# Kernel tuning notes

Measured on AMD Instinct MI355X. Metric: run time of the kernel, lower is better.

The kernel has to match this reference:

```python
import jax, jax.numpy as jnp
import numpy as np

T, E, D, F, K, CAP = 4096, 8, 1024, 4096, 2, 1024


def setup_inputs() -> dict:
    key = jax.random.key(0)
    ks = jax.random.split(key, 4)
    x = jax.random.normal(ks[0], (T, D), jnp.float32)
    # top-k routing: mask/weight consistent with a softmax router
    logits = jax.random.normal(ks[1], (T, E), jnp.float32)
    probs = jax.nn.softmax(logits, axis=-1)
    _, topi = jax.lax.top_k(probs, K)  # (T, K)
    route_mask = jnp.zeros((T, E), jnp.bool_).at[jnp.arange(T)[:, None], topi].set(True)
    route_weight = jnp.where(route_mask, probs, 0.0)
    # stacked expert MLP params (E leading axis, as ModuleGroup stacks them)
    w1 = jax.random.normal(ks[2], (E, D, F), jnp.float32) * 0.02
    b1 = jnp.zeros((E, F), jnp.float32)
    w2 = jax.random.normal(ks[3], (E, F, D), jnp.float32) * 0.02
    b2 = jnp.zeros((E, D), jnp.float32)
    return dict(x=x, route_mask=route_mask, route_weight=route_weight,
                w1=w1, b1=b1, w2=w2, b2=b2)


def _build_slots(mask_te, w_te, cap):
    # mask_te: (T,E) bool; w_te: (T,E) float (0 where unrouted)
    Tn, En = mask_te.shape
    m_et = mask_te.T                              # (E,T)
    w_et = jnp.where(m_et, w_te.T, -jnp.inf)      # unrouted -> -inf
    _, idx_top = jax.lax.top_k(w_et, cap)         # (E,C) token ids per slot
    slot = jnp.zeros((En, cap, Tn), w_te.dtype)
    slot = slot.at[jnp.arange(En)[:, None], jnp.arange(cap)[None, :], idx_top].set(1.0)
    slot = slot * m_et[:, None, :].astype(w_te.dtype)  # zero slots from -inf picks
    # NOTE: the original re-orders slots along C (a stable sort); the combine
    # einsum sums over C so the output is invariant to slot order -- skipped.
    return slot


def reference(x, route_mask, route_weight, w1, b1, w2, b2):
    w_te = jnp.where(route_mask, route_weight, 0.0)      # (T,E)
    slot = _build_slots(route_mask, w_te, CAP)           # (E,C,T) one-hot
    # dispatch: 'ect,t...->ec...'
    xs = jnp.einsum('ect,td->ecd', slot, x)              # (E,C,D)
    # expert compute (vmapped MLP over E)
    h = jax.nn.gelu(jnp.einsum('ecd,edf->ecf', xs, w1) + b1[:, None, :])
    out = jnp.einsum('ecf,efd->ecd', h, w2) + b2[:, None, :]
    # combine: 'ecf,ect,te->tf'
    y = jnp.einsum('ecd,ect,te->td', out, slot, w_te)    # (T,D)
    return y
```

## Files before the change

kernel.cpp:

```cpp
#include <hip/hip_runtime.h>
#include <hip/hip_bf16.h>
#include <stdint.h>

#define T_TOK 4096
#define E_EXP 8
#define D_DIM 1024
#define F_DIM 4096
#define K_TOP 2
#define CAPC  1024

typedef __attribute__((ext_vector_type(8))) short short8;
typedef __attribute__((ext_vector_type(4))) float f32x4;
typedef __attribute__((ext_vector_type(4))) unsigned short u16x4;

static __device__ __forceinline__ unsigned short f2bf(float f) {
  union { float f; unsigned u; } v; v.f = f;
  unsigned r = v.u + 0x7fffu + ((v.u >> 16) & 1u);
  return (unsigned short)(r >> 16);
}

static __device__ __forceinline__ void gload_lds16(const void* g, void* l) {
  __builtin_amdgcn_global_load_lds(
      (const __attribute__((address_space(1))) unsigned int*)g,
      (__attribute__((address_space(3))) unsigned int*)l, 16, 0, 0);
}

__global__ void zero_int_kernel(int* p, int n) {
  int i = blockIdx.x * 256 + threadIdx.x;
  if (i < n) p[i] = 0;
}

__global__ __launch_bounds__(1024) void select_kernel(
    const float* __restrict__ rw,
    int* __restrict__ sel_idx,
    int* __restrict__ inv_cnt,
    int* __restrict__ inv_ec,
    float* __restrict__ inv_w)
{
  __shared__ unsigned keys[T_TOK];
  __shared__ int hist[256];
  __shared__ int scan_s[1024];
  __shared__ int sh_need;
  __shared__ unsigned sh_prefix;
  __shared__ int slot_ctr;
  const int e = blockIdx.x;
  const int tid = threadIdx.x;

  if (tid < CAPC) sel_idx[e * CAPC + tid] = -1;
#pragma unroll
  for (int j = 0; j < 4; ++j) {
    int t = tid * 4 + j;
    float w = rw[(size_t)t * E_EXP + e];
    keys[t] = (w > 0.f) ? __float_as_uint(w) : 0u;
  }
  if (tid == 0) slot_ctr = 0;

  int need = CAPC;
  unsigned prefix = 0;
  for (int shift = 24; shift >= 0; shift -= 8) {
    __syncthreads();
    if (tid < 256) hist[tid] = 0;
    __syncthreads();
#pragma unroll
    for (int j = 0; j < 4; ++j) {
      unsigned k = keys[tid * 4 + j];
      unsigned hi = (shift == 24) ? 0u : (k >> (shift + 8));
      if (hi == prefix) atomicAdd(&hist[(k >> shift) & 255u], 1);
    }
    __syncthreads();
    if (tid == 0) {
      int cum = 0, b = 0;
      for (b = 255; b >= 0; --b) {
        cum += hist[b];
        if (cum >= need) break;
      }
      if (b < 0) b = 0;
      sh_need = need - (cum - hist[b]);
      sh_prefix = (prefix << 8) | (unsigned)b;
    }
    __syncthreads();
    need = sh_need;
    prefix = sh_prefix;
  }
  const unsigned thr = prefix;
  __syncthreads();

  int eqflag[4], myeq = 0;
#pragma unroll
  for (int j = 0; j < 4; ++j) {
    const int t = tid * 4 + j;
    const unsigned k = keys[t];
    if (k > thr) {
      int s = atomicAdd(&slot_ctr, 1);
      sel_idx[e * CAPC + s] = t;
      int p = atomicAdd(&inv_cnt[t], 1);
      inv_ec[t * K_TOP + p] = e * CAPC + s;
      inv_w[t * K_TOP + p] = __uint_as_float(k);
    }
    eqflag[j] = (thr > 0u && k == thr) ? 1 : 0;
    myeq += eqflag[j];
  }
  scan_s[tid] = myeq;
  __syncthreads();
  for (int d = 1; d < 1024; d <<= 1) {
    int v = scan_s[tid];
    int add = (tid >= d) ? scan_s[tid - d] : 0;
    __syncthreads();
    scan_s[tid] = v + add;
    __syncthreads();
  }
  int r = scan_s[tid] - myeq;
  const int base = CAPC - need;
#pragma unroll
  for (int j = 0; j < 4; ++j) {
    if (eqflag[j]) {
      if (r < need) {
        const int t = tid * 4 + j;
        const int s = base + r;
        sel_idx[e * CAPC + s] = t;
        int p = atomicAdd(&inv_cnt[t], 1);
        inv_ec[t * K_TOP + p] = e * CAPC + s;
        inv_w[t * K_TOP + p] = __uint_as_float(thr);
      }
      ++r;
    }
  }
}

__global__ void convert_x_kernel(const float* __restrict__ x,
                                 unsigned short* __restrict__ xb, int n4) {
  int i = blockIdx.x * 256 + threadIdx.x;
  if (i >= n4) return;
  f32x4 v = ((const f32x4*)x)[i];
  u16x4 o = { f2bf(v.x), f2bf(v.y), f2bf(v.z), f2bf(v.w) };
  ((u16x4*)xb)[i] = o;
}

__global__ __launch_bounds__(256) void transpose_bf16_kernel(
    const float* __restrict__ in, unsigned short* __restrict__ out,
    int R, int C)
{
  __shared__ unsigned short tile[64][68];
  const int e = blockIdx.z;
  const float* inp = in + (size_t)e * R * C;
  unsigned short* outp = out + (size_t)e * R * C;
  const int c0 = blockIdx.x * 64, r0 = blockIdx.y * 64;
  const int q4 = (threadIdx.x & 15) * 4;
  const int tr = threadIdx.x >> 4;
  for (int rr = tr; rr < 64; rr += 16) {
    f32x4 v = *(const f32x4*)(inp + (size_t)(r0 + rr) * C + c0 + q4);
    tile[rr][q4 + 0] = f2bf(v.x);
    tile[rr][q4 + 1] = f2bf(v.y);
    tile[rr][q4 + 2] = f2bf(v.z);
    tile[rr][q4 + 3] = f2bf(v.w);
  }
  __syncthreads();
  for (int cc = tr; cc < 64; cc += 16) {
    u16x4 o = { tile[q4 + 0][cc], tile[q4 + 1][cc],
                tile[q4 + 2][cc], tile[q4 + 3][cc] };
    *(u16x4*)(outp + (size_t)(c0 + cc) * R + r0 + q4) = o;
  }
}


__global__ __launch_bounds__(256, 3) void gemm1_kernel(
    const unsigned short* __restrict__ xb,
    const int* __restrict__ sel_idx,
    const unsigned short* __restrict__ w1t,
    const float* __restrict__ b1,
    unsigned short* __restrict__ H)
{
  const int lin = blockIdx.x + 32 * (blockIdx.y + 8 * blockIdx.z);
  const int e = lin & 7;
  const int slot = lin >> 3;
  const int xb_ = slot >> 3;
  const int yb_ = slot & 7;
  const int m0 = yb_ * 128;
  const int n0 = xb_ * 128;

  __shared__ __align__(16) unsigned short Asm[128 * 64];
  __shared__ __align__(16) unsigned short Bsm[128 * 64];
  const int tid = threadIdx.x;
  const int lane = tid & 63, wv = tid >> 6;
  const int wm = (wv >> 1) * 64, wn = (wv & 1) * 64;
  const int lrow = lane & 15, quad = lane >> 4;

  const int rbase = tid >> 3, seg = tid & 7;
  const int cs = seg ^ (rbase & 7);
  const unsigned short* gA[4];
  const unsigned short* gB[4];
  char* lA[4];
  char* lB[4];
  const unsigned short* w1e = w1t + (size_t)e * F_DIM * D_DIM;
#pragma unroll
  for (int it = 0; it < 4; ++it) {
    const int row = rbase + it * 32;
    int t = sel_idx[e * CAPC + m0 + row];
    if (t < 0) t = 0;
    gA[it] = xb + (size_t)t * D_DIM + cs * 8;
    gB[it] = w1e + (size_t)(n0 + row) * D_DIM + cs * 8;
    lA[it] = (char*)Asm + it * 4096 + wv * 1024;
    lB[it] = (char*)Bsm + it * 4096 + wv * 1024;
  }

  f32x4 acc[4][4];
#pragma unroll
  for (int a = 0; a < 4; ++a)
#pragma unroll
    for (int b = 0; b < 4; ++b) acc[a][b] = (f32x4){0.f, 0.f, 0.f, 0.f};

  const int sw = lrow & 7;
  for (int k0 = 0; k0 < D_DIM; k0 += 64) {
#pragma unroll
    for (int it = 0; it < 4; ++it) { gload_lds16(gA[it], lA[it]); gA[it] += 64; }
#pragma unroll
    for (int it = 0; it < 4; ++it) { gload_lds16(gB[it], lB[it]); gB[it] += 64; }
    __syncthreads();
#pragma unroll
    for (int h = 0; h < 2; ++h) {
      short8 af[4], bf[4];
#pragma unroll
      for (int mt = 0; mt < 4; ++mt)
        af[mt] = *(const short8*)(Asm + (wm + mt * 16 + lrow) * 64 +
                                  (((h << 2) + quad) ^ sw) * 8);
#pragma unroll
      for (int nt = 0; nt < 4; ++nt)
        bf[nt] = *(const short8*)(Bsm + (wn + nt * 16 + lrow) * 64 +
                                  (((h << 2) + quad) ^ sw) * 8);
#pragma unroll
      for (int mt = 0; mt < 4; ++mt)
#pragma unroll
        for (int nt = 0; nt < 4; ++nt)
          acc[mt][nt] = __builtin_amdgcn_mfma_f32_16x16x32_bf16(
              af[mt], bf[nt], acc[mt][nt], 0, 0, 0);
    }
    __syncthreads();
  }

  const float* b1e = b1 + e * F_DIM;
#pragma unroll
  for (int nt = 0; nt < 4; ++nt) {
    const int col = n0 + wn + nt * 16 + lrow;
    const float bias = b1e[col];
#pragma unroll
    for (int mt = 0; mt < 4; ++mt) {
      const int rowb = m0 + wm + mt * 16 + quad * 4;
#pragma unroll
      for (int i = 0; i < 4; ++i) {
        float v = acc[mt][nt][i] + bias;
        float u = 0.7978845608028654f * (v + 0.044715f * v * v * v);
        float th = 1.f - 2.f / (1.f + __expf(2.f * u));
        float hv = 0.5f * v * (1.f + th);
        H[((size_t)e * CAPC + rowb + i) * F_DIM + col] = f2bf(hv);
      }
    }
  }
}

__global__ __launch_bounds__(256, 3) void gemm2_kernel(
    const unsigned short* __restrict__ H,
    const unsigned short* __restrict__ w2t,
    const float* __restrict__ b2,
    float* __restrict__ P)
{
  const int lin = blockIdx.x + 8 * (blockIdx.y + 8 * blockIdx.z);
  const int xcd = lin & 7;
  const int slot = lin >> 3;
  const int g = xcd * 2 + (slot >> 6);
  const int e = g & 7;
  const int ks = g >> 3;
  const int tile = slot & 63;
  const int xb_ = tile >> 3;
  const int yb_ = tile & 7;
  const int m0 = yb_ * 128;
  const int n0 = xb_ * 128;
  const int kbase = ks * (F_DIM / 2);

  __shared__ __align__(16) unsigned short Asm[128 * 64];
  __shared__ __align__(16) unsigned short Bsm[128 * 64];
  const int tid = threadIdx.x;
  const int lane = tid & 63, wv = tid >> 6;
  const int wm = (wv >> 1) * 64, wn = (wv & 1) * 64;
  const int lrow = lane & 15, quad = lane >> 4;

  const int rbase = tid >> 3, seg = tid & 7;
  const int cs = seg ^ (rbase & 7);
  const unsigned short* gA[4];
  const unsigned short* gB[4];
  char* lA[4];
  char* lB[4];
  const unsigned short* He = H + (size_t)e * CAPC * F_DIM;
  const unsigned short* w2e = w2t + (size_t)e * D_DIM * F_DIM;
#pragma unroll
  for (int it = 0; it < 4; ++it) {
    const int row = rbase + it * 32;
    gA[it] = He + (size_t)(m0 + row) * F_DIM + kbase + cs * 8;
    gB[it] = w2e + (size_t)(n0 + row) * F_DIM + kbase + cs * 8;
    lA[it] = (char*)Asm + it * 4096 + wv * 1024;
    lB[it] = (char*)Bsm + it * 4096 + wv * 1024;
  }

  f32x4 acc[4][4];
#pragma unroll
  for (int a = 0; a < 4; ++a)
#pragma unroll
    for (int b = 0; b < 4; ++b) acc[a][b] = (f32x4){0.f, 0.f, 0.f, 0.f};

  const int sw = lrow & 7;
  for (int k0 = 0; k0 < F_DIM / 2; k0 += 64) {
#pragma unroll
    for (int it = 0; it < 4; ++it) { gload_lds16(gA[it], lA[it]); gA[it] += 64; }
#pragma unroll
    for (int it = 0; it < 4; ++it) { gload_lds16(gB[it], lB[it]); gB[it] += 64; }
    __syncthreads();
#pragma unroll
    for (int h = 0; h < 2; ++h) {
      short8 af[4], bf[4];
#pragma unroll
      for (int mt = 0; mt < 4; ++mt)
        af[mt] = *(const short8*)(Asm + (wm + mt * 16 + lrow) * 64 +
                                  (((h << 2) + quad) ^ sw) * 8);
#pragma unroll
      for (int nt = 0; nt < 4; ++nt)
        bf[nt] = *(const short8*)(Bsm + (wn + nt * 16 + lrow) * 64 +
                                  (((h << 2) + quad) ^ sw) * 8);
#pragma unroll
      for (int mt = 0; mt < 4; ++mt)
#pragma unroll
        for (int nt = 0; nt < 4; ++nt)
          acc[mt][nt] = __builtin_amdgcn_mfma_f32_16x16x32_bf16(
              af[mt], bf[nt], acc[mt][nt], 0, 0, 0);
    }
    __syncthreads();
  }

  const float* b2e = b2 + e * D_DIM;
  float* Pk = P + (size_t)ks * E_EXP * CAPC * D_DIM;
#pragma unroll
  for (int nt = 0; nt < 4; ++nt) {
    const int col = n0 + wn + nt * 16 + lrow;
    const float bias = (ks == 0) ? b2e[col] : 0.f;
#pragma unroll
    for (int mt = 0; mt < 4; ++mt) {
      const int rowb = m0 + wm + mt * 16 + quad * 4;
#pragma unroll
      for (int i = 0; i < 4; ++i) {
        Pk[((size_t)e * CAPC + rowb + i) * D_DIM + col] = acc[mt][nt][i] + bias;
      }
    }
  }
}

__global__ __launch_bounds__(256) void combine_kernel(
    const float* __restrict__ P, const int* __restrict__ inv_cnt,
    const int* __restrict__ inv_ec, const float* __restrict__ inv_w,
    float* __restrict__ y)
{
  const int t = blockIdx.x;
  const int cnt = inv_cnt[t];
  f32x4 s = {0.f, 0.f, 0.f, 0.f};
  const int d4 = threadIdx.x;
  const size_t half = (size_t)E_EXP * CAPC * D_DIM;
  for (int p = 0; p < cnt; ++p) {
    const int ec = inv_ec[t * K_TOP + p];
    const float w = inv_w[t * K_TOP + p];
    f32x4 v0 = ((const f32x4*)(P + (size_t)ec * D_DIM))[d4];
    f32x4 v1 = ((const f32x4*)(P + half + (size_t)ec * D_DIM))[d4];
    s += (v0 + v1) * w;
  }
  ((f32x4*)(y + (size_t)t * D_DIM))[d4] = s;
}

extern "C" void kernel_launch(void* const* d_in, const int* in_sizes, int n_in,
                              void* d_out, int out_size, void* d_ws, size_t ws_size,
                              hipStream_t stream) {
  (void)in_sizes; (void)n_in; (void)out_size; (void)ws_size;
  const float* x  = (const float*)d_in[0];
  const float* rw = (const float*)d_in[2];
  const float* w1 = (const float*)d_in[3];
  const float* b1 = (const float*)d_in[4];
  const float* w2 = (const float*)d_in[5];
  const float* b2 = (const float*)d_in[6];
  float* y = (float*)d_out;

  char* ws = (char*)d_ws;
  size_t off = 0;
  auto alloc = [&](size_t bytes) {
    void* p = ws + off;
    off += (bytes + 255) & ~(size_t)255;
    return p;
  };
  unsigned short* xb  = (unsigned short*)alloc((size_t)T_TOK * D_DIM * 2);
  unsigned short* w1t = (unsigned short*)alloc((size_t)E_EXP * F_DIM * D_DIM * 2);
  unsigned short* w2t = (unsigned short*)alloc((size_t)E_EXP * D_DIM * F_DIM * 2);
  unsigned short* H   = (unsigned short*)alloc((size_t)E_EXP * CAPC * F_DIM * 2);
  float* P            = (float*)alloc((size_t)2 * E_EXP * CAPC * D_DIM * 4);
  int* sel_idx        = (int*)alloc((size_t)E_EXP * CAPC * 4);
  int* inv_cnt        = (int*)alloc((size_t)T_TOK * 4);
  int* inv_ec         = (int*)alloc((size_t)T_TOK * K_TOP * 4);
  float* inv_w        = (float*)alloc((size_t)T_TOK * K_TOP * 4);

  zero_int_kernel<<<(T_TOK + 255) / 256, 256, 0, stream>>>(inv_cnt, T_TOK);
  select_kernel<<<E_EXP, 1024, 0, stream>>>(rw, sel_idx, inv_cnt, inv_ec, inv_w);

  convert_x_kernel<<<(T_TOK * D_DIM / 4 + 255) / 256, 256, 0, stream>>>(
      x, xb, T_TOK * D_DIM / 4);
  transpose_bf16_kernel<<<dim3(F_DIM / 64, D_DIM / 64, E_EXP), 256, 0, stream>>>(
      w1, w1t, D_DIM, F_DIM);
  transpose_bf16_kernel<<<dim3(D_DIM / 64, F_DIM / 64, E_EXP), 256, 0, stream>>>(
      w2, w2t, F_DIM, D_DIM);

  gemm1_kernel<<<dim3(F_DIM / 128, CAPC / 128, E_EXP), 256, 0, stream>>>(
      xb, sel_idx, w1t, b1, H);
  gemm2_kernel<<<dim3(D_DIM / 128, CAPC / 128, E_EXP * 2), 256, 0, stream>>>(
      H, w2t, b2, P);

  combine_kernel<<<T_TOK, 256, 0, stream>>>(P, inv_cnt, inv_ec, inv_w, y);
}
```

Measured before the change: 612.3 us.

## Fuse routing select, x conversion and weight transposes into one prep kernel

Merges the per-expert top-capacity selection, the x fp32-to-bf16 conversion and both weight transpose-converts into a single block-partitioned prep kernel. This cuts launch count and lets the small 8-block select overlap with the bandwidth-heavy conversion work. The transpose now uses 128x64 tiles with packed 32-bit LDS writes and 16-byte global stores. The XCD-aware block remapping in both GEMMs is replaced by plain blockIdx indexing, which may change L2 locality. The select path drops from 1024 to 256 threads, so each thread handles 16 keys.

```diff
diff --git a/kernel.cpp b/kernel.cpp
--- a/kernel.cpp
+++ b/kernel.cpp
@@ -12,6 +12,7 @@
 typedef __attribute__((ext_vector_type(8))) short short8;
 typedef __attribute__((ext_vector_type(4))) float f32x4;
 typedef __attribute__((ext_vector_type(4))) unsigned short u16x4;
+typedef __attribute__((ext_vector_type(8))) unsigned short u16x8;
 
 static __device__ __forceinline__ unsigned short f2bf(float f) {
   union { float f; unsigned u; } v; v.f = f;
@@ -30,27 +31,83 @@
   if (i < n) p[i] = 0;
 }
 
-__global__ __launch_bounds__(1024) void select_kernel(
+#define PREP_SEL0   0
+#define PREP_CVT0   8
+#define PREP_TR0    4104
+#define PREP_NBLK   12296
+
+__global__ __launch_bounds__(256) void prep_kernel(
+    const float* __restrict__ x,
     const float* __restrict__ rw,
+    const float* __restrict__ w1,
+    const float* __restrict__ w2,
+    unsigned short* __restrict__ xb,
+    unsigned short* __restrict__ w1t,
+    unsigned short* __restrict__ w2t,
     int* __restrict__ sel_idx,
     int* __restrict__ inv_cnt,
     int* __restrict__ inv_ec,
     float* __restrict__ inv_w)
 {
-  __shared__ unsigned keys[T_TOK];
-  __shared__ int hist[256];
-  __shared__ int scan_s[1024];
+  __shared__ __align__(16) char smem[18560];
   __shared__ int sh_need;
   __shared__ unsigned sh_prefix;
   __shared__ int slot_ctr;
-  const int e = blockIdx.x;
+  const int bid = blockIdx.x;
   const int tid = threadIdx.x;
 
-  if (tid < CAPC) sel_idx[e * CAPC + tid] = -1;
-#pragma unroll
-  for (int j = 0; j < 4; ++j) {
-    int t = tid * 4 + j;
-    float w = rw[(size_t)t * E_EXP + e];
+  if (bid >= PREP_TR0) {
+    const int tb = bid - PREP_TR0;
+    const float* inp; unsigned short* outp; int R, C, r0, c0;
+    if (tb < 4096) {
+      const int e = tb >> 9, ti = tb & 511;
+      R = 1024; C = 4096;
+      r0 = (ti & 7) * 128; c0 = (ti >> 3) * 64;
+      inp = w1 + (size_t)e * R * C; outp = w1t + (size_t)e * R * C;
+    } else {
+      const int t2 = tb - 4096, e = t2 >> 9, ti = t2 & 511;
+      R = 4096; C = 1024;
+      r0 = (ti & 31) * 128; c0 = (ti >> 5) * 64;
+      inp = w2 + (size_t)e * R * C; outp = w2t + (size_t)e * R * C;
+    }
+    unsigned short* tile = (unsigned short*)smem;
+    const int q4 = (tid & 15) * 4, tr = tid >> 4;
+    for (int rr = tr; rr < 128; rr += 16) {
+      f32x4 v = *(const f32x4*)(inp + (size_t)(r0 + rr) * C + c0 + q4);
+      unsigned* t32 = (unsigned*)(tile + rr * 66 + q4);
+      t32[0] = (unsigned)f2bf(v.x) | ((unsigned)f2bf(v.y) << 16);
+      t32[1] = (unsigned)f2bf(v.z) | ((unsigned)f2bf(v.w) << 16);
+    }
+    __syncthreads();
+    const int l = tid & 15, ccb = tid >> 4;
+#pragma unroll
+    for (int it = 0; it < 4; ++it) {
+      const int cc = ccb + it * 16;
+      u16x8 o;
+#pragma unroll
+      for (int j = 0; j < 8; ++j) o[j] = tile[(l * 8 + j) * 66 + cc];
+      *(u16x8*)(outp + (size_t)(c0 + cc) * R + r0 + l * 8) = o;
+    }
+    return;
+  }
+
+  if (bid >= PREP_CVT0) {
+    const int i = (bid - PREP_CVT0) * 256 + tid;
+    f32x4 v = ((const f32x4*)x)[i];
+    u16x4 o = { f2bf(v.x), f2bf(v.y), f2bf(v.z), f2bf(v.w) };
+    ((u16x4*)xb)[i] = o;
+    return;
+  }
+
+  unsigned* keys = (unsigned*)smem;
+  int* hist = (int*)(smem + 16384);
+  int* scn  = (int*)(smem + 16384 + 1024);
+  const int e = bid;
+  for (int c = tid; c < CAPC; c += 256) sel_idx[e * CAPC + c] = -1;
+#pragma unroll
+  for (int j = 0; j < 16; ++j) {
+    const int t = tid * 16 + j;
+    const float w = rw[(size_t)t * E_EXP + e];
     keys[t] = (w > 0.f) ? __float_as_uint(w) : 0u;
   }
   if (tid == 0) slot_ctr = 0;
@@ -59,17 +116,17 @@
   unsigned prefix = 0;
   for (int shift = 24; shift >= 0; shift -= 8) {
     __syncthreads();
-    if (tid < 256) hist[tid] = 0;
-    __syncthreads();
-#pragma unroll
-    for (int j = 0; j < 4; ++j) {
-      unsigned k = keys[tid * 4 + j];
-      unsigned hi = (shift == 24) ? 0u : (k >> (shift + 8));
+    hist[tid] = 0;
+    __syncthreads();
+#pragma unroll
+    for (int j = 0; j < 16; ++j) {
+      const unsigned k = keys[tid * 16 + j];
+      const unsigned hi = (shift == 24) ? 0u : (k >> (shift + 8));
       if (hi == prefix) atomicAdd(&hist[(k >> shift) & 255u], 1);
     }
     __syncthreads();
     if (tid == 0) {
-      int cum = 0, b = 0;
+      int cum = 0, b;
       for (b = 255; b >= 0; --b) {
         cum += hist[b];
         if (cum >= need) break;
@@ -85,80 +142,44 @@
   const unsigned thr = prefix;
   __syncthreads();
 
-  int eqflag[4], myeq = 0;
-#pragma unroll
-  for (int j = 0; j < 4; ++j) {
-    const int t = tid * 4 + j;
+  int eqbits = 0, myeq = 0;
+#pragma unroll
+  for (int j = 0; j < 16; ++j) {
+    const int t = tid * 16 + j;
     const unsigned k = keys[t];
     if (k > thr) {
-      int s = atomicAdd(&slot_ctr, 1);
+      const int s = atomicAdd(&slot_ctr, 1);
       sel_idx[e * CAPC + s] = t;
-      int p = atomicAdd(&inv_cnt[t], 1);
+      const int p = atomicAdd(&inv_cnt[t], 1);
       inv_ec[t * K_TOP + p] = e * CAPC + s;
       inv_w[t * K_TOP + p] = __uint_as_float(k);
     }
-    eqflag[j] = (thr > 0u && k == thr) ? 1 : 0;
-    myeq += eqflag[j];
-  }
-  scan_s[tid] = myeq;
+    if (thr > 0u && k == thr) { eqbits |= (1 << j); ++myeq; }
+  }
+  scn[tid] = myeq;
   __syncthreads();
-  for (int d = 1; d < 1024; d <<= 1) {
-    int v = scan_s[tid];
-    int add = (tid >= d) ? scan_s[tid - d] : 0;
-    __syncthreads();
-    scan_s[tid] = v + add;
-    __syncthreads();
-  }
-  int r = scan_s[tid] - myeq;
+  for (int d = 1; d < 256; d <<= 1) {
+    const int v = scn[tid];
+    const int a = (tid >= d) ? scn[tid - d] : 0;
+    __syncthreads();
+    scn[tid] = v + a;
+    __syncthreads();
+  }
+  int r = scn[tid] - myeq;
   const int base = CAPC - need;
 #pragma unroll
-  for (int j = 0; j < 4; ++j) {
-    if (eqflag[j]) {
+  for (int j = 0; j < 16; ++j) {
+    if ((eqbits >> j) & 1) {
       if (r < need) {
-        const int t = tid * 4 + j;
+        const int t = tid * 16 + j;
         const int s = base + r;
         sel_idx[e * CAPC + s] = t;
-        int p = atomicAdd(&inv_cnt[t], 1);
+        const int p = atomicAdd(&inv_cnt[t], 1);
         inv_ec[t * K_TOP + p] = e * CAPC + s;
         inv_w[t * K_TOP + p] = __uint_as_float(thr);
       }
       ++r;
     }
-  }
-}
-
-__global__ void convert_x_kernel(const float* __restrict__ x,
-                                 unsigned short* __restrict__ xb, int n4) {
-  int i = blockIdx.x * 256 + threadIdx.x;
-  if (i >= n4) return;
-  f32x4 v = ((const f32x4*)x)[i];
-  u16x4 o = { f2bf(v.x), f2bf(v.y), f2bf(v.z), f2bf(v.w) };
-  ((u16x4*)xb)[i] = o;
-}
-
-__global__ __launch_bounds__(256) void transpose_bf16_kernel(
-    const float* __restrict__ in, unsigned short* __restrict__ out,
-    int R, int C)
-{
-  __shared__ unsigned short tile[64][68];
-  const int e = blockIdx.z;
-  const float* inp = in + (size_t)e * R * C;
-  unsigned short* outp = out + (size_t)e * R * C;
-  const int c0 = blockIdx.x * 64, r0 = blockIdx.y * 64;
-  const int q4 = (threadIdx.x & 15) * 4;
-  const int tr = threadIdx.x >> 4;
-  for (int rr = tr; rr < 64; rr += 16) {
-    f32x4 v = *(const f32x4*)(inp + (size_t)(r0 + rr) * C + c0 + q4);
-    tile[rr][q4 + 0] = f2bf(v.x);
-    tile[rr][q4 + 1] = f2bf(v.y);
-    tile[rr][q4 + 2] = f2bf(v.z);
-    tile[rr][q4 + 3] = f2bf(v.w);
-  }
-  __syncthreads();
-  for (int cc = tr; cc < 64; cc += 16) {
-    u16x4 o = { tile[q4 + 0][cc], tile[q4 + 1][cc],
-                tile[q4 + 2][cc], tile[q4 + 3][cc] };
-    *(u16x4*)(outp + (size_t)(c0 + cc) * R + r0 + q4) = o;
   }
 }
 
@@ -170,16 +191,11 @@
     const float* __restrict__ b1,
     unsigned short* __restrict__ H)
 {
-  const int lin = blockIdx.x + 32 * (blockIdx.y + 8 * blockIdx.z);
-  const int e = lin & 7;
-  const int slot = lin >> 3;
-  const int xb_ = slot >> 3;
-  const int yb_ = slot & 7;
-  const int m0 = yb_ * 128;
-  const int n0 = xb_ * 128;
-
   __shared__ __align__(16) unsigned short Asm[128 * 64];
   __shared__ __align__(16) unsigned short Bsm[128 * 64];
+  const int e = blockIdx.z;
+  const int m0 = blockIdx.y * 128;
+  const int n0 = blockIdx.x * 128;
   const int tid = threadIdx.x;
   const int lane = tid & 63, wv = tid >> 6;
   const int wm = (wv >> 1) * 64, wn = (wv & 1) * 64;
@@ -263,21 +279,13 @@
     const float* __restrict__ b2,
     float* __restrict__ P)
 {
-  const int lin = blockIdx.x + 8 * (blockIdx.y + 8 * blockIdx.z);
-  const int xcd = lin & 7;
-  const int slot = lin >> 3;
-  const int g = xcd * 2 + (slot >> 6);
-  const int e = g & 7;
-  const int ks = g >> 3;
-  const int tile = slot & 63;
-  const int xb_ = tile >> 3;
-  const int yb_ = tile & 7;
-  const int m0 = yb_ * 128;
-  const int n0 = xb_ * 128;
-  const int kbase = ks * (F_DIM / 2);
-
   __shared__ __align__(16) unsigned short Asm[128 * 64];
   __shared__ __align__(16) unsigned short Bsm[128 * 64];
+  const int e = blockIdx.z & 7;
+  const int ks = blockIdx.z >> 3;
+  const int m0 = blockIdx.y * 128;
+  const int n0 = blockIdx.x * 128;
+  const int kbase = ks * (F_DIM / 2);
   const int tid = threadIdx.x;
   const int lane = tid & 63, wv = tid >> 6;
   const int wm = (wv >> 1) * 64, wn = (wv & 1) * 64;
@@ -401,14 +409,9 @@
   float* inv_w        = (float*)alloc((size_t)T_TOK * K_TOP * 4);
 
   zero_int_kernel<<<(T_TOK + 255) / 256, 256, 0, stream>>>(inv_cnt, T_TOK);
-  select_kernel<<<E_EXP, 1024, 0, stream>>>(rw, sel_idx, inv_cnt, inv_ec, inv_w);
-
-  convert_x_kernel<<<(T_TOK * D_DIM / 4 + 255) / 256, 256, 0, stream>>>(
-      x, xb, T_TOK * D_DIM / 4);
-  transpose_bf16_kernel<<<dim3(F_DIM / 64, D_DIM / 64, E_EXP), 256, 0, stream>>>(
-      w1, w1t, D_DIM, F_DIM);
-  transpose_bf16_kernel<<<dim3(D_DIM / 64, F_DIM / 64, E_EXP), 256, 0, stream>>>(
-      w2, w2t, F_DIM, D_DIM);
+
+  prep_kernel<<<PREP_NBLK, 256, 0, stream>>>(
+      x, rw, w1, w2, xb, w1t, w2t, sel_idx, inv_cnt, inv_ec, inv_w);
 
   gemm1_kernel<<<dim3(F_DIM / 128, CAPC / 128, E_EXP), 256, 0, stream>>>(
       xb, sel_idx, w1t, b1, H);
```

After: 534.4 us. 1.15x faster.
